# Kernel tuning notes

Hardware: AMD Instinct MI355X
Metric: run time of the kernel (lower is better)

## Reference

```python
import jax, jax.numpy as jnp
import numpy as np

N_NODES = 100000
N_EDGES = 1600000
NEG_SLOPE = 0.2  # PyG GATConv default


def _glorot(key, shape):
    fan = sum(shape[:2]) if len(shape) > 1 else shape[0] * 2
    s = jnp.sqrt(6.0 / fan)
    return jax.random.uniform(key, shape, jnp.float32, -s, s)


def gat_layer(x, src, dst, edge_attr, W, a_src, a_dst, We, a_e, b, heads, out_ch, concat):
    """Faithful PyG GATConv (add_self_loops=True, fill_value='mean', edge_dim set)."""
    n = x.shape[0]
    # self-loop edge_attr = mean of incoming edge_attr per dst node (0 if none)
    deg = jax.ops.segment_sum(jnp.ones((src.shape[0],), edge_attr.dtype), dst, num_segments=n)
    loop_attr = jax.ops.segment_sum(edge_attr, dst, num_segments=n) / jnp.maximum(deg, 1.0)[:, None]
    loop = jnp.arange(n, dtype=src.dtype)
    src_f = jnp.concatenate([src, loop])
    dst_f = jnp.concatenate([dst, loop])
    ea = jnp.concatenate([edge_attr, loop_attr], axis=0)
    # node transform -> [n, H, C]
    h = (x @ W).reshape(n, heads, out_ch)
    al_src = jnp.sum(h * a_src, axis=-1)  # [n, H]
    al_dst = jnp.sum(h * a_dst, axis=-1)  # [n, H]
    e = (ea @ We).reshape(-1, heads, out_ch)
    al_e = jnp.sum(e * a_e, axis=-1)      # [Ef, H]
    alpha = jax.nn.leaky_relu(al_src[src_f] + al_dst[dst_f] + al_e, negative_slope=NEG_SLOPE)
    # segment softmax over destination nodes (every node has a self loop)
    m = jax.ops.segment_max(alpha, dst_f, num_segments=n)
    ex = jnp.exp(alpha - m[dst_f])
    den = jax.ops.segment_sum(ex, dst_f, num_segments=n)
    att = ex / den[dst_f]                 # [Ef, H]
    out = jax.ops.segment_sum(att[:, :, None] * h[src_f], dst_f, num_segments=n)  # [n, H, C]
    out = out.reshape(n, heads * out_ch) if concat else out.mean(axis=1)
    return out + b


def setup_inputs() -> dict:
    key = jax.random.key(0)
    ks = jax.random.split(key, 20)
    x = jax.random.normal(ks[0], (N_NODES, 5), jnp.float32)
    edge_index = jax.random.randint(ks[1], (2, N_EDGES), 0, N_NODES, jnp.int64)
    edge_attr = jax.random.normal(ks[2], (N_EDGES, 2), jnp.float32)
    # conv1: in=5, out=32, heads=4, concat -> 128
    p = {
        "W1": _glorot(ks[3], (5, 128)), "aS1": _glorot(ks[4], (4, 32)),
        "aD1": _glorot(ks[5], (4, 32)), "We1": _glorot(ks[6], (2, 128)),
        "aE1": _glorot(ks[7], (4, 32)), "b1": jnp.zeros((128,), jnp.float32),
        # conv2: in=128, out=32, heads=2, concat -> 64
        "W2": _glorot(ks[8], (128, 64)), "aS2": _glorot(ks[9], (2, 32)),
        "aD2": _glorot(ks[10], (2, 32)), "We2": _glorot(ks[11], (2, 64)),
        "aE2": _glorot(ks[12], (2, 32)), "b2": jnp.zeros((64,), jnp.float32),
        # conv3: in=64, out=1, heads=1, concat=False
        "W3": _glorot(ks[13], (64, 1)), "aS3": _glorot(ks[14], (1, 1)),
        "aD3": _glorot(ks[15], (1, 1)), "We3": _glorot(ks[16], (2, 1)),
        "aE3": _glorot(ks[17], (1, 1)), "b3": jnp.zeros((1,), jnp.float32),
    }
    return {"x": x, "edge_index": edge_index, "edge_attr": edge_attr, **p}


def reference(x, edge_index, edge_attr,
              W1, aS1, aD1, We1, aE1, b1,
              W2, aS2, aD2, We2, aE2, b2,
              W3, aS3, aD3, We3, aE3, b3):
    src, dst = edge_index[0], edge_index[1]
    h = gat_layer(x, src, dst, edge_attr, W1, aS1, aD1, We1, aE1, b1, 4, 32, True)
    h = jax.nn.elu(h)  # dropout is identity in eval
    h = gat_layer(h, src, dst, edge_attr, W2, aS2, aD2, We2, aE2, b2, 2, 32, True)
    h = jax.nn.elu(h)
    h = gat_layer(h, src, dst, edge_attr, W3, aS3, aD3, We3, aE3, b3, 1, 1, False)
    return jax.nn.sigmoid(h).squeeze(-1)  # [N]
```

## Files before the change

### kernel.cpp

```cpp
#include <hip/hip_runtime.h>
#include <math.h>

#define NN 100000
#define NE 1600000
#define NPB 256
#define NPB_SHIFT 8
#define NB ((NN + NPB - 1) / NPB)
#define NCHUNK 512
#define CH ((NE + NCHUNK - 1) / NCHUNK)
#define LOG2E 1.44269504088896f

typedef __attribute__((ext_vector_type(8))) short short8v;
typedef __attribute__((ext_vector_type(4))) float f32x4;

__device__ __forceinline__ float lrelu(float x) { return fmaxf(x, 0.2f * x); }
__device__ __forceinline__ float elu1(float x) { return x > 0.f ? x : (__expf(x) - 1.f); }
__device__ __forceinline__ float fexp2(float x) {
#if __has_builtin(__builtin_amdgcn_exp2f)
    return __builtin_amdgcn_exp2f(x);
#else
    return exp2f(x);
#endif
}
__device__ __forceinline__ unsigned bf16rne(float f) {
    unsigned u = __float_as_uint(f);
    return (u + 0x7FFFu + ((u >> 16) & 1u)) >> 16;
}
__device__ __forceinline__ float bf16lo(unsigned u) { return __uint_as_float(u << 16); }
__device__ __forceinline__ float bf16hi(unsigned u) {
    return __uint_as_float(u & 0xFFFF0000u);
}
__device__ __forceinline__ void split2(float x0, float x1, unsigned& hp, unsigned& lp) {
    unsigned h0 = bf16rne(x0), h1 = bf16rne(x1);
    float r0 = x0 - __uint_as_float(h0 << 16);
    float r1 = x1 - __uint_as_float(h1 << 16);
    hp = h0 | (h1 << 16);
    lp = bf16rne(r0) | (bf16rne(r1) << 16);
}

__global__ void __launch_bounds__(256) k_binA0(const int* __restrict__ dst,
                                               int* __restrict__ bucket_cnt) {
    __shared__ int hist[NB];
    int t = threadIdx.x;
    for (int b = t; b < NB; b += 256) hist[b] = 0;
    __syncthreads();
    int c0 = blockIdx.x * CH, c1 = min(NE, c0 + CH);
    for (int e = c0 + t; e < c1; e += 256) atomicAdd(&hist[dst[e] >> NPB_SHIFT], 1);
    __syncthreads();
    for (int b = t; b < NB; b += 256)
        if (hist[b]) atomicAdd(&bucket_cnt[b], hist[b]);
}

__global__ void __launch_bounds__(512) k_bscan(const int* __restrict__ bucket_cnt,
                                               int* __restrict__ bucket_base,
                                               int* __restrict__ bucket_tail) {
    __shared__ int s[512];
    int t = threadIdx.x;
    int v = (t < NB) ? bucket_cnt[t] : 0;
    s[t] = v;
    __syncthreads();
    for (int off = 1; off < 512; off <<= 1) {
        int x = (t >= off) ? s[t - off] : 0;
        __syncthreads();
        if (t >= off) s[t] += x;
        __syncthreads();
    }
    if (t < NB) {
        int ex = s[t] - v;
        bucket_base[t] = ex;
        bucket_tail[t] = ex;
        if (t == NB - 1) bucket_base[NB] = s[t];
    }
}

__global__ void __launch_bounds__(256) k_binA2(const int* __restrict__ src,
                                               const int* __restrict__ dst,
                                               const float* __restrict__ ea,
                                               int* __restrict__ bucket_tail,
                                               uint2* __restrict__ binned,
                                               unsigned char* __restrict__ dstb) {
    __shared__ int hist[NB], pre[NB], cursor[NB], base_l[NB];
    __shared__ int psum[256];
    __shared__ uint2 lrec[CH];
    __shared__ int lds_d[CH];
    int t = threadIdx.x;
    for (int b = t; b < NB; b += 256) hist[b] = 0;
    __syncthreads();
    int c0 = blockIdx.x * CH, c1 = min(NE, c0 + CH);
    int cnt = c1 - c0;
    for (int i = t; i < cnt; i += 256) atomicAdd(&hist[dst[c0 + i] >> NPB_SHIFT], 1);
    __syncthreads();
    int b0 = t << 1, b1 = b0 + 1;
    int h0 = (b0 < NB) ? hist[b0] : 0;
    int h1 = (b1 < NB) ? hist[b1] : 0;
    psum[t] = h0 + h1;
    __syncthreads();
    for (int off = 1; off < 256; off <<= 1) {
        int x = (t >= off) ? psum[t - off] : 0;
        __syncthreads();
        if (t >= off) psum[t] += x;
        __syncthreads();
    }
    int ex = psum[t] - (h0 + h1);
    if (b0 < NB) { pre[b0] = ex;      cursor[b0] = ex; }
    if (b1 < NB) { pre[b1] = ex + h0; cursor[b1] = ex + h0; }
    for (int b = t; b < NB; b += 256) {
        int h = hist[b];
        if (h) base_l[b] = atomicAdd(&bucket_tail[b], h);
    }
    __syncthreads();
    for (int i = t; i < cnt; i += 256) {
        int e = c0 + i;
        int d = dst[e];
        int bkt = d >> NPB_SHIFT;
        int lpos = atomicAdd(&cursor[bkt], 1);
        unsigned pk = bf16rne(ea[2 * e]) | (bf16rne(ea[2 * e + 1]) << 16);
        lrec[lpos] = make_uint2((unsigned)src[e], pk);
        lds_d[lpos] = d;
    }
    __syncthreads();
    for (int i = t; i < cnt; i += 256) {
        int d = lds_d[i];
        int bkt = d >> NPB_SHIFT;
        int gpos = base_l[bkt] + (i - pre[bkt]);
        binned[gpos] = lrec[i];
        dstb[gpos] = (unsigned char)(d & (NPB - 1));
    }
}

__global__ void __launch_bounds__(256) k_binB(const int* __restrict__ bucket_base,
                                              const uint2* __restrict__ binned,
                                              const unsigned char* __restrict__ dstb,
                                              int* __restrict__ rowptr,
                                              uint2* __restrict__ edges,
                                              float* __restrict__ la) {
    __shared__ int hist[NPB], pre[NPB], cursor[NPB];
    __shared__ float ea0s[NPB], ea1s[NPB];
    int b = blockIdx.x, t = threadIdx.x;
    int bb = bucket_base[b], be = bucket_base[b + 1];
    int nb0 = b << NPB_SHIFT;
    hist[t] = 0;
    ea0s[t] = 0.f;
    ea1s[t] = 0.f;
    __syncthreads();
    for (int e = bb + t; e < be; e += 256) atomicAdd(&hist[dstb[e]], 1);
    __syncthreads();
    int v = hist[t];
    pre[t] = v;
    __syncthreads();
    for (int off = 1; off < 256; off <<= 1) {
        int x = (t >= off) ? pre[t - off] : 0;
        __syncthreads();
        if (t >= off) pre[t] += x;
        __syncthreads();
    }
    int ex = pre[t] - v;
    if (nb0 + t <= NN) rowptr[nb0 + t] = bb + ex;
    cursor[t] = bb + ex;
    __syncthreads();
    for (int e = bb + t; e < be; e += 256) {
        uint2 rec = binned[e];
        unsigned char d = dstb[e];
        int pos = atomicAdd(&cursor[d], 1);
        edges[pos] = rec;
        atomicAdd(&ea0s[d], bf16lo(rec.y));
        atomicAdd(&ea1s[d], bf16hi(rec.y));
    }
    __syncthreads();
    int n = nb0 + t;
    if (n < NN) {
        float dg = fmaxf((float)v, 1.0f);
        la[2 * n] = ea0s[t] / dg;
        la[2 * n + 1] = ea1s[t] / dg;
    }
}

__global__ void k_const(const float* __restrict__ We1, const float* __restrict__ aE1,
                        const float* __restrict__ We2, const float* __restrict__ aE2,
                        const float* __restrict__ We3, const float* __restrict__ aE3,
                        const float* __restrict__ W1, const float* __restrict__ aS1,
                        const float* __restrict__ aD1, float* __restrict__ cbuf) {
    int t = threadIdx.x;
    if (t < 8) {
        int d = t >> 2, hd = t & 3;
        float s = 0.f;
        for (int c = 0; c < 32; c++) s += We1[d * 128 + hd * 32 + c] * aE1[hd * 32 + c];
        cbuf[t] = s * LOG2E;
    } else if (t < 12) {
        int idx = t - 8, d = idx >> 1, hd = idx & 1;
        float s = 0.f;
        for (int c = 0; c < 32; c++) s += We2[d * 64 + hd * 32 + c] * aE2[hd * 32 + c];
        cbuf[t] = s * LOG2E;
    } else if (t < 14) {
        cbuf[t] = We3[t - 12] * aE3[0] * LOG2E;
    } else if (t >= 16 && t < 56) {
        int r = (t - 16) % 20, hd = r / 5, i = r % 5;
        const float* a = (t - 16 < 20) ? aS1 : aD1;
        float s = 0.f;
        for (int c = 0; c < 32; c++) s += W1[i * 128 + hd * 32 + c] * a[hd * 32 + c];
        cbuf[t] = s * LOG2E;
    }
}

__global__ void k_w2t(const float* __restrict__ W2, unsigned short* __restrict__ W2th,
                      unsigned short* __restrict__ W2tl) {
    int i = blockIdx.x * 256 + threadIdx.x;
    if (i >= 64 * 128) return;
    int c = i >> 7, k = i & 127;
    float v = W2[k * 64 + c];
    unsigned h = bf16rne(v);
    float hf = __uint_as_float(h << 16);
    unsigned lo = bf16rne(v - hf);
    W2th[c * 128 + k] = (unsigned short)h;
    W2tl[c * 128 + k] = (unsigned short)lo;
}

__global__ void k_prep1(const float* __restrict__ x, const float* __restrict__ vsd,
                        float4* __restrict__ xp, float4* __restrict__ als1,
                        float4* __restrict__ ald1) {
    int n = blockIdx.x * blockDim.x + threadIdx.x;
    if (n >= NN) return;
    float x0 = x[5 * n], x1 = x[5 * n + 1], x2 = x[5 * n + 2], x3 = x[5 * n + 3],
          x4 = x[5 * n + 4];
    xp[2 * n] = make_float4(x0, x1, x2, x3);
    xp[2 * n + 1] = make_float4(x4, 0.f, 0.f, 0.f);
    float sv[4], dv[4];
#pragma unroll
    for (int hd = 0; hd < 4; hd++) {
        const float* vS = vsd + hd * 5;
        const float* vD = vsd + 20 + hd * 5;
        sv[hd] = x0 * vS[0] + x1 * vS[1] + x2 * vS[2] + x3 * vS[3] + x4 * vS[4];
        dv[hd] = x0 * vD[0] + x1 * vD[1] + x2 * vD[2] + x3 * vD[3] + x4 * vD[4];
    }
    als1[n] = make_float4(sv[0], sv[1], sv[2], sv[3]);
    ald1[n] = make_float4(dv[0], dv[1], dv[2], dv[3]);
}

__global__ void k_agg1(const int* __restrict__ rowptr, const uint2* __restrict__ edges,
                       const float4* __restrict__ xp, const float* __restrict__ als1,
                       const float* __restrict__ ald1, const float* __restrict__ la,
                       const float* __restrict__ me, float* __restrict__ xw) {
    int t = blockIdx.x * blockDim.x + threadIdx.x;
    if (t >= NN * 4) return;
    int n = t >> 2, hd = t & 3;
    float me0 = me[hd], me1 = me[4 + hd];
    float aldn = ald1[t];
    float aself = lrelu(als1[t] + aldn + la[2 * n] * me0 + la[2 * n + 1] * me1);
    int start = rowptr[n], end = rowptr[n + 1];
    float den = 1.f;
    float4 xa = xp[2 * n];
    float xb = xp[2 * n + 1].x;
    float a0 = xa.x, a1 = xa.y, a2 = xa.z, a3 = xa.w, a4 = xb;
    int e = start;
    if ((e & 1) && e < end) {
        uint2 ep = edges[e];
        int s = (int)ep.x;
        float a = lrelu(als1[s * 4 + hd] + aldn + bf16lo(ep.y) * me0 + bf16hi(ep.y) * me1);
        float p = fexp2(a - aself);
        den += p;
        float4 sa = xp[2 * s];
        float sb = xp[2 * s + 1].x;
        a0 += p * sa.x; a1 += p * sa.y; a2 += p * sa.z; a3 += p * sa.w; a4 += p * sb;
        e++;
    }
    for (; e + 1 < end; e += 2) {
        uint4 two = *(const uint4*)(edges + e);
        int s0 = (int)two.x, s1 = (int)two.z;
        unsigned pk0 = two.y, pk1 = two.w;
        float l0 = als1[s0 * 4 + hd];
        float l1 = als1[s1 * 4 + hd];
        float4 sa0 = xp[2 * s0];
        float sb0 = xp[2 * s0 + 1].x;
        float4 sa1 = xp[2 * s1];
        float sb1 = xp[2 * s1 + 1].x;
        float av0 = lrelu(l0 + aldn + bf16lo(pk0) * me0 + bf16hi(pk0) * me1);
        float av1 = lrelu(l1 + aldn + bf16lo(pk1) * me0 + bf16hi(pk1) * me1);
        float p0 = fexp2(av0 - aself);
        float p1 = fexp2(av1 - aself);
        den += p0 + p1;
        a0 += p0 * sa0.x + p1 * sa1.x;
        a1 += p0 * sa0.y + p1 * sa1.y;
        a2 += p0 * sa0.z + p1 * sa1.z;
        a3 += p0 * sa0.w + p1 * sa1.w;
        a4 += p0 * sb0 + p1 * sb1;
    }
    if (e < end) {
        uint2 ep = edges[e];
        int s = (int)ep.x;
        float a = lrelu(als1[s * 4 + hd] + aldn + bf16lo(ep.y) * me0 + bf16hi(ep.y) * me1);
        float p = fexp2(a - aself);
        den += p;
        float4 sa = xp[2 * s];
        float sb = xp[2 * s + 1].x;
        a0 += p * sa.x; a1 += p * sa.y; a2 += p * sa.z; a3 += p * sa.w; a4 += p * sb;
    }
    float r = 1.f / den;
    float* w = xw + (size_t)n * 20 + hd * 5;
    w[0] = a0 * r;
    w[1] = a1 * r;
    w[2] = a2 * r;
    w[3] = a3 * r;
    w[4] = a4 * r;
}

__global__ void __launch_bounds__(128) k_l2trans(
        const float* __restrict__ xw, const float* __restrict__ W1,
        const float* __restrict__ b1, const unsigned short* __restrict__ W2th,
        const unsigned short* __restrict__ W2tl,
        const float* __restrict__ aS2, const float* __restrict__ aD2,
        unsigned short* __restrict__ h2q, float* __restrict__ als2,
        float* __restrict__ ald2) {
    __shared__ float wstage[32 * 20];
    __shared__ unsigned short Ahi[4096];
    __shared__ unsigned short Alo[4096];
    int nb = blockIdx.x * 32, t = threadIdx.x;
    {
        int base = nb * 20;
        for (int idx = t; idx < 32 * 20; idx += 128) wstage[idx] = xw[base + idx];
    }
    __syncthreads();
    {
        int nl = t >> 2, g = t & 3;
        int w = nl >> 4, row = nl & 15;
#pragma unroll
        for (int kt = 0; kt < 4; ++kt) {
            int ch0 = kt * 32 + g * 8;
            float4 va = *(const float4*)(b1 + ch0);
            float4 vb = *(const float4*)(b1 + ch0 + 4);
            const float* wp = wstage + nl * 20 + kt * 5;
#pragma unroll
            for (int i = 0; i < 5; ++i) {
                float wi = wp[i];
                float4 A = *(const float4*)(W1 + i * 128 + ch0);
                float4 B = *(const float4*)(W1 + i * 128 + ch0 + 4);
                va.x += wi * A.x; va.y += wi * A.y; va.z += wi * A.z; va.w += wi * A.w;
                vb.x += wi * B.x; vb.y += wi * B.y; vb.z += wi * B.z; vb.w += wi * B.w;
            }
            unsigned hp0, hp1, hp2, hp3, lp0, lp1, lp2, lp3;
            split2(elu1(va.x), elu1(va.y), hp0, lp0);
            split2(elu1(va.z), elu1(va.w), hp1, lp1);
            split2(elu1(vb.x), elu1(vb.y), hp2, lp2);
            split2(elu1(vb.z), elu1(vb.w), hp3, lp3);
            int cidx = (((w * 4 + kt) * 64) + g * 16 + row) * 8;
            *(uint4*)(Ahi + cidx) = make_uint4(hp0, hp1, hp2, hp3);
            *(uint4*)(Alo + cidx) = make_uint4(lp0, lp1, lp2, lp3);
        }
    }
    int l = t & 63, w = t >> 6;
    int g = l >> 4, row16 = l & 15;
    f32x4 acc0 = {0.f, 0.f, 0.f, 0.f}, acc1 = acc0, acc2 = acc0, acc3 = acc0;
    int w4 = w * 4;
#pragma unroll
    for (int kt = 0; kt < 4; ++kt) {
        int abase = ((w4 + kt) * 64 + l) * 8;
        short8v ah = *(const short8v*)(Ahi + abase);
        short8v al = *(const short8v*)(Alo + abase);
        int kb = kt * 32 + g * 8;
        {
            short8v bh = *(const short8v*)(W2th + row16 * 128 + kb);
            short8v bl = *(const short8v*)(W2tl + row16 * 128 + kb);
            acc0 = __builtin_amdgcn_mfma_f32_16x16x32_bf16(ah, bh, acc0, 0, 0, 0);
            acc0 = __builtin_amdgcn_mfma_f32_16x16x32_bf16(al, bh, acc0, 0, 0, 0);
            acc0 = __builtin_amdgcn_mfma_f32_16x16x32_bf16(ah, bl, acc0, 0, 0, 0);
        }
        {
            short8v bh = *(const short8v*)(W2th + (16 + row16) * 128 + kb);
            short8v bl = *(const short8v*)(W2tl + (16 + row16) * 128 + kb);
            acc1 = __builtin_amdgcn_mfma_f32_16x16x32_bf16(ah, bh, acc1, 0, 0, 0);
            acc1 = __builtin_amdgcn_mfma_f32_16x16x32_bf16(al, bh, acc1, 0, 0, 0);
            acc1 = __builtin_amdgcn_mfma_f32_16x16x32_bf16(ah, bl, acc1, 0, 0, 0);
        }
        {
            short8v bh = *(const short8v*)(W2th + (32 + row16) * 128 + kb);
            short8v bl = *(const short8v*)(W2tl + (32 + row16) * 128 + kb);
            acc2 = __builtin_amdgcn_mfma_f32_16x16x32_bf16(ah, bh, acc2, 0, 0, 0);
            acc2 = __builtin_amdgcn_mfma_f32_16x16x32_bf16(al, bh, acc2, 0, 0, 0);
            acc2 = __builtin_amdgcn_mfma_f32_16x16x32_bf16(ah, bl, acc2, 0, 0, 0);
        }
        {
            short8v bh = *(const short8v*)(W2th + (48 + row16) * 128 + kb);
            short8v bl = *(const short8v*)(W2tl + (48 + row16) * 128 + kb);
            acc3 = __builtin_amdgcn_mfma_f32_16x16x32_bf16(ah, bh, acc3, 0, 0, 0);
            acc3 = __builtin_amdgcn_mfma_f32_16x16x32_bf16(al, bh, acc3, 0, 0, 0);
            acc3 = __builtin_amdgcn_mfma_f32_16x16x32_bf16(ah, bl, acc3, 0, 0, 0);
        }
    }
    {
        int nodeb = nb + w * 16 + g * 4;
#pragma unroll
        for (int nt = 0; nt < 4; ++nt) {
            f32x4 A = (nt == 0) ? acc0 : (nt == 1) ? acc1 : (nt == 2) ? acc2 : acc3;
#pragma unroll
            for (int r = 0; r < 4; ++r) {
                float v = A[r];
                float u = __shfl_xor(v, 1);
                if (!(l & 1)) {
                    unsigned pk = bf16rne(v) | (bf16rne(u) << 16);
                    int node = nodeb + r;
                    int ch = nt * 16 + row16;
                    *(unsigned*)(h2q + (size_t)node * 64 + ch) = pk;
                }
            }
        }
        float aSv0 = aS2[row16], aSv1 = aS2[16 + row16];
        float aSv2 = aS2[32 + row16], aSv3 = aS2[48 + row16];
        float aDv0 = aD2[row16], aDv1 = aD2[16 + row16];
        float aDv2 = aD2[32 + row16], aDv3 = aD2[48 + row16];
#pragma unroll
        for (int r = 0; r < 4; ++r) {
            float pS0 = acc0[r] * aSv0 + acc1[r] * aSv1;
            float pS1 = acc2[r] * aSv2 + acc3[r] * aSv3;
            float pD0 = acc0[r] * aDv0 + acc1[r] * aDv1;
            float pD1 = acc2[r] * aDv2 + acc3[r] * aDv3;
#pragma unroll
            for (int off = 1; off < 16; off <<= 1) {
                pS0 += __shfl_xor(pS0, off);
                pS1 += __shfl_xor(pS1, off);
                pD0 += __shfl_xor(pD0, off);
                pD1 += __shfl_xor(pD1, off);
            }
            if (row16 == 0) {
                int node = nodeb + r;
                als2[node * 2 + 0] = pS0 * LOG2E;
                als2[node * 2 + 1] = pS1 * LOG2E;
                ald2[node * 2 + 0] = pD0 * LOG2E;
                ald2[node * 2 + 1] = pD1 * LOG2E;
            }
        }
    }
}

#define AGG2_EDGE(u0, u1, p)                                            \
    acc[0] += (p) * bf16lo(u0.x); acc[1] += (p) * bf16hi(u0.x);         \
    acc[2] += (p) * bf16lo(u0.y); acc[3] += (p) * bf16hi(u0.y);         \
    acc[4] += (p) * bf16lo(u0.z); acc[5] += (p) * bf16hi(u0.z);         \
    acc[6] += (p) * bf16lo(u0.w); acc[7] += (p) * bf16hi(u0.w);         \
    acc[8] += (p) * bf16lo(u1.x); acc[9] += (p) * bf16hi(u1.x);         \
    acc[10] += (p) * bf16lo(u1.y); acc[11] += (p) * bf16hi(u1.y);       \
    acc[12] += (p) * bf16lo(u1.z); acc[13] += (p) * bf16hi(u1.z);       \
    acc[14] += (p) * bf16lo(u1.w); acc[15] += (p) * bf16hi(u1.w);

__global__ void k_agg2(const int* __restrict__ rowptr, const uint2* __restrict__ edges,
                       const unsigned short* __restrict__ h2q,
                       const float* __restrict__ als2, const float* __restrict__ ald2,
                       const float* __restrict__ la, const float* __restrict__ me,
                       const float* __restrict__ b2, const float* __restrict__ W3,
                       float* __restrict__ h3) {
    int t = blockIdx.x * blockDim.x + threadIdx.x;
    if (t >= NN * 4) return;
    int n = t >> 2, sub = t & 3, hd = sub >> 1, qh = sub & 1;
    int cbase = hd * 32 + qh * 16;
    float me0 = me[hd], me1 = me[2 + hd];
    float aldn = ald2[n * 2 + hd];
    float aself = lrelu(als2[n * 2 + hd] + aldn + la[2 * n] * me0 + la[2 * n + 1] * me1);
    int start = rowptr[n], end = rowptr[n + 1];
    float den = 1.f;
    float acc[16];
    {
        const uint4* hp = (const uint4*)(h2q + (size_t)n * 64 + cbase);
        uint4 u0 = hp[0], u1 = hp[1];
        acc[0] = bf16lo(u0.x); acc[1] = bf16hi(u0.x);
        acc[2] = bf16lo(u0.y); acc[3] = bf16hi(u0.y);
        acc[4] = bf16lo(u0.z); acc[5] = bf16hi(u0.z);
        acc[6] = bf16lo(u0.w); acc[7] = bf16hi(u0.w);
        acc[8] = bf16lo(u1.x); acc[9] = bf16hi(u1.x);
        acc[10] = bf16lo(u1.y); acc[11] = bf16hi(u1.y);
        acc[12] = bf16lo(u1.z); acc[13] = bf16hi(u1.z);
        acc[14] = bf16lo(u1.w); acc[15] = bf16hi(u1.w);
    }
    int e = start;
    if ((e & 1) && e < end) {
        uint2 ep = edges[e];
        int s = (int)ep.x;
        float a = lrelu(als2[s * 2 + hd] + aldn + bf16lo(ep.y) * me0 + bf16hi(ep.y) * me1);
        float p = fexp2(a - aself);
        den += p;
        const uint4* sp = (const uint4*)(h2q + (size_t)s * 64 + cbase);
        uint4 u0 = sp[0], u1 = sp[1];
        AGG2_EDGE(u0, u1, p)
        e++;
    }
    for (; e + 3 < end; e += 4) {
        uint4 twoA = *(const uint4*)(edges + e);
        uint4 twoB = *(const uint4*)(edges + e + 2);
        int s0 = (int)twoA.x, s1 = (int)twoA.z;
        int s2 = (int)twoB.x, s3 = (int)twoB.z;
        float l0 = als2[s0 * 2 + hd];
        float l1 = als2[s1 * 2 + hd];
        float l2 = als2[s2 * 2 + hd];
        float l3 = als2[s3 * 2 + hd];
        const uint4* sp0 = (const uint4*)(h2q + (size_t)s0 * 64 + cbase);
        const uint4* sp1 = (const uint4*)(h2q + (size_t)s1 * 64 + cbase);
        const uint4* sp2 = (const uint4*)(h2q + (size_t)s2 * 64 + cbase);
        const uint4* sp3 = (const uint4*)(h2q + (size_t)s3 * 64 + cbase);
        uint4 u00 = sp0[0], u01 = sp0[1];
        uint4 u10 = sp1[0], u11 = sp1[1];
        uint4 u20 = sp2[0], u21 = sp2[1];
        uint4 u30 = sp3[0], u31 = sp3[1];
        float av0 = lrelu(l0 + aldn + bf16lo(twoA.y) * me0 + bf16hi(twoA.y) * me1);
        float av1 = lrelu(l1 + aldn + bf16lo(twoA.w) * me0 + bf16hi(twoA.w) * me1);
        float av2 = lrelu(l2 + aldn + bf16lo(twoB.y) * me0 + bf16hi(twoB.y) * me1);
        float av3 = lrelu(l3 + aldn + bf16lo(twoB.w) * me0 + bf16hi(twoB.w) * me1);
        float p0 = fexp2(av0 - aself);
        float p1 = fexp2(av1 - aself);
        float p2 = fexp2(av2 - aself);
        float p3 = fexp2(av3 - aself);
        den += (p0 + p1) + (p2 + p3);
        acc[0] += p0 * bf16lo(u00.x) + p1 * bf16lo(u10.x) + p2 * bf16lo(u20.x) + p3 * bf16lo(u30.x);
        acc[1] += p0 * bf16hi(u00.x) + p1 * bf16hi(u10.x) + p2 * bf16hi(u20.x) + p3 * bf16hi(u30.x);
        acc[2] += p0 * bf16lo(u00.y) + p1 * bf16lo(u10.y) + p2 * bf16lo(u20.y) + p3 * bf16lo(u30.y);
        acc[3] += p0 * bf16hi(u00.y) + p1 * bf16hi(u10.y) + p2 * bf16hi(u20.y) + p3 * bf16hi(u30.y);
        acc[4] += p0 * bf16lo(u00.z) + p1 * bf16lo(u10.z) + p2 * bf16lo(u20.z) + p3 * bf16lo(u30.z);
        acc[5] += p0 * bf16hi(u00.z) + p1 * bf16hi(u10.z) + p2 * bf16hi(u20.z) + p3 * bf16hi(u30.z);
        acc[6] += p0 * bf16lo(u00.w) + p1 * bf16lo(u10.w) + p2 * bf16lo(u20.w) + p3 * bf16lo(u30.w);
        acc[7] += p0 * bf16hi(u00.w) + p1 * bf16hi(u10.w) + p2 * bf16hi(u20.w) + p3 * bf16hi(u30.w);
        acc[8] += p0 * bf16lo(u01.x) + p1 * bf16lo(u11.x) + p2 * bf16lo(u21.x) + p3 * bf16lo(u31.x);
        acc[9] += p0 * bf16hi(u01.x) + p1 * bf16hi(u11.x) + p2 * bf16hi(u21.x) + p3 * bf16hi(u31.x);
        acc[10] += p0 * bf16lo(u01.y) + p1 * bf16lo(u11.y) + p2 * bf16lo(u21.y) + p3 * bf16lo(u31.y);
        acc[11] += p0 * bf16hi(u01.y) + p1 * bf16hi(u11.y) + p2 * bf16hi(u21.y) + p3 * bf16hi(u31.y);
        acc[12] += p0 * bf16lo(u01.z) + p1 * bf16lo(u11.z) + p2 * bf16lo(u21.z) + p3 * bf16lo(u31.z);
        acc[13] += p0 * bf16hi(u01.z) + p1 * bf16hi(u11.z) + p2 * bf16hi(u21.z) + p3 * bf16hi(u31.z);
        acc[14] += p0 * bf16lo(u01.w) + p1 * bf16lo(u11.w) + p2 * bf16lo(u21.w) + p3 * bf16lo(u31.w);
        acc[15] += p0 * bf16hi(u01.w) + p1 * bf16hi(u11.w) + p2 * bf16hi(u21.w) + p3 * bf16hi(u31.w);
    }
    if (e + 1 < end) {
        uint4 two = *(const uint4*)(edges + e);
        int s0 = (int)two.x, s1 = (int)two.z;
        float l0 = als2[s0 * 2 + hd];
        float l1 = als2[s1 * 2 + hd];
        const uint4* sp0 = (const uint4*)(h2q + (size_t)s0 * 64 + cbase);
        const uint4* sp1 = (const uint4*)(h2q + (size_t)s1 * 64 + cbase);
        uint4 u00 = sp0[0], u01 = sp0[1];
        uint4 u10 = sp1[0], u11 = sp1[1];
        float av0 = lrelu(l0 + aldn + bf16lo(two.y) * me0 + bf16hi(two.y) * me1);
        float av1 = lrelu(l1 + aldn + bf16lo(two.w) * me0 + bf16hi(two.w) * me1);
        float p0 = fexp2(av0 - aself);
        float p1 = fexp2(av1 - aself);
        den += p0 + p1;
        AGG2_EDGE(u00, u01, p0)
        AGG2_EDGE(u10, u11, p1)
        e += 2;
    }
    if (e < end) {
        uint2 ep = edges[e];
        int s = (int)ep.x;
        float a = lrelu(als2[s * 2 + hd] + aldn + bf16lo(ep.y) * me0 + bf16hi(ep.y) * me1);
        float p = fexp2(a - aself);
        den += p;
        const uint4* sp = (const uint4*)(h2q + (size_t)s * 64 + cbase);
        uint4 u0 = sp[0], u1 = sp[1];
        AGG2_EDGE(u0, u1, p)
    }
    float r = 1.f / den;
    float part = 0.f;
#pragma unroll
    for (int c = 0; c < 16; c++) {
        float v = elu1(acc[c] * r + b2[cbase + c]);
        part += v * W3[cbase + c];
    }
    part += __shfl_xor(part, 1);
    part += __shfl_xor(part, 2);
    if (sub == 0) h3[n] = part;
}

__global__ void k_agg3(const int* __restrict__ rowptr, const uint2* __restrict__ edges,
                       const float* __restrict__ h, const float* __restrict__ aS3,
                       const float* __restrict__ aD3, const float* __restrict__ la,
                       const float* __restrict__ me, const float* __restrict__ b,
                       float* __restrict__ out) {
    int tid = blockIdx.x * blockDim.x + threadIdx.x;
    int n = tid >> 4;
    if (n >= NN) return;
    int lane = tid & 15;
    float me0 = me[0], me1 = me[1];
    float aSs = aS3[0] * LOG2E, aDs = aD3[0] * LOG2E;
    float hn = h[n];
    float ald_n = hn * aDs;
    float aself = lrelu(hn * aSs + ald_n + la[2 * n] * me0 + la[2 * n + 1] * me1);
    int start = rowptr[n], end = rowptr[n + 1];
    float den = 0.f, num = 0.f;
    for (int e = start + lane; e < end; e += 16) {
        uint2 ep = edges[e];
        int s = (int)ep.x;
        float hv = h[s];
        float a = lrelu(hv * aSs + ald_n + bf16lo(ep.y) * me0 + bf16hi(ep.y) * me1);
        float p = fexp2(a - aself);
        den += p;
        num += p * hv;
    }
#pragma unroll
    for (int off = 8; off > 0; off >>= 1) {
        den += __shfl_xor(den, off);
        num += __shfl_xor(num, off);
    }
    if (lane == 0) {
        den += 1.f;
        num += hn;
        float v = num / den + b[0];
        out[n] = 1.f / (1.f + __expf(-v));
    }
}

extern "C" void kernel_launch(void* const* d_in, const int* in_sizes, int n_in,
                              void* d_out, int out_size, void* d_ws, size_t ws_size,
                              hipStream_t stream) {
    const float* x   = (const float*)d_in[0];
    const int*   ei  = (const int*)d_in[1];
    const float* ea  = (const float*)d_in[2];
    const float* W1  = (const float*)d_in[3];
    const float* aS1 = (const float*)d_in[4];
    const float* aD1 = (const float*)d_in[5];
    const float* We1 = (const float*)d_in[6];
    const float* aE1 = (const float*)d_in[7];
    const float* b1  = (const float*)d_in[8];
    const float* W2  = (const float*)d_in[9];
    const float* aS2 = (const float*)d_in[10];
    const float* aD2 = (const float*)d_in[11];
    const float* We2 = (const float*)d_in[12];
    const float* aE2 = (const float*)d_in[13];
    const float* b2  = (const float*)d_in[14];
    const float* W3  = (const float*)d_in[15];
    const float* aS3 = (const float*)d_in[16];
    const float* aD3 = (const float*)d_in[17];
    const float* We3 = (const float*)d_in[18];
    const float* aE3 = (const float*)d_in[19];
    const float* b3  = (const float*)d_in[20];

    const int* srcv = ei;
    const int* dstv = ei + NE;

    char* basep = (char*)d_ws;
    size_t off = 0;
    auto alloc = [&](size_t nbytes) -> void* {
        void* p = basep + off;
        off += (nbytes + 255) & ~(size_t)255;
        return p;
    };
    int*    bucket_cnt  = (int*)alloc((size_t)(NB + 1) * 4);
    int*    bucket_base = (int*)alloc((size_t)(NB + 1) * 4);
    int*    bucket_tail = (int*)alloc((size_t)(NB + 1) * 4);
    int*    rowptr      = (int*)alloc((size_t)(NN + 1) * 4);
    uint2*  binned      = (uint2*)alloc((size_t)NE * 8);
    unsigned char* dstb = (unsigned char*)alloc((size_t)NE);
    uint2*  edges       = (uint2*)alloc((size_t)NE * 8);
    float*  la          = (float*)alloc((size_t)NN * 8);
    float*  cbuf        = (float*)alloc(256);
    float4* xp          = (float4*)alloc((size_t)NN * 32);
    float4* als1        = (float4*)alloc((size_t)NN * 16);
    float4* ald1        = (float4*)alloc((size_t)NN * 16);
    float*  xw          = (float*)alloc((size_t)NN * 80);
    unsigned short* h2q = (unsigned short*)alloc((size_t)NN * 128);
    float*  als2        = (float*)alloc((size_t)NN * 8);
    float*  ald2        = (float*)alloc((size_t)NN * 8);
    float*  h3          = (float*)alloc((size_t)NN * 4);
    unsigned short* W2th = (unsigned short*)alloc(64 * 128 * 2);
    unsigned short* W2tl = (unsigned short*)alloc(64 * 128 * 2);
    (void)ws_size; (void)in_sizes; (void)n_in; (void)out_size;

    float* me1 = cbuf;
    float* me2 = cbuf + 8;
    float* me3 = cbuf + 12;
    float* vsd = cbuf + 16;

    auto cdiv = [](long long a, long long b) { return (int)((a + b - 1) / b); };
    const int BS = 256;

    hipMemsetAsync(bucket_cnt, 0, (size_t)(NB + 1) * 4, stream);
    k_binA0<<<NCHUNK, 256, 0, stream>>>(dstv, bucket_cnt);
    k_bscan<<<1, 512, 0, stream>>>(bucket_cnt, bucket_base, bucket_tail);
    k_binA2<<<NCHUNK, 256, 0, stream>>>(srcv, dstv, ea, bucket_tail, binned, dstb);
    k_binB<<<NB, 256, 0, stream>>>(bucket_base, binned, dstb, rowptr, edges, la);

    k_const<<<1, 64, 0, stream>>>(We1, aE1, We2, aE2, We3, aE3, W1, aS1, aD1, cbuf);
    k_w2t<<<32, 256, 0, stream>>>(W2, W2th, W2tl);

    k_prep1<<<cdiv(NN, BS), BS, 0, stream>>>(x, vsd, xp, als1, ald1);
    k_agg1<<<cdiv((long long)NN * 4, BS), BS, 0, stream>>>(rowptr, edges, xp,
                                                           (const float*)als1,
                                                           (const float*)ald1, la, me1, xw);

    k_l2trans<<<cdiv(NN, 32), 128, 0, stream>>>(xw, W1, b1, W2th, W2tl, aS2, aD2,
                                                h2q, als2, ald2);
    k_agg2<<<cdiv((long long)NN * 4, BS), BS, 0, stream>>>(rowptr, edges, h2q, als2, ald2,
                                                           la, me2, b2, W3, h3);

    k_agg3<<<cdiv((long long)NN * 16, BS), BS, 0, stream>>>(rowptr, edges, h3, aS3, aD3,
                                                            la, me3, b3, (float*)d_out);
}
```

Baseline: 320.8 us.

## Fuse layer-1 W1 transform and ELU into aggregation, write MFMA-ready tiles to global

The layer-1 aggregation kernel now applies the W1 projection, bias, ELU and hi/lo bf16 split directly after computing each node-head's aggregated features. It writes the result in the MFMA fragment layout to global buffers. A separate lean MFMA kernel then loads those fragments to produce h2 and the layer-2 attention logits. This removes the intermediate xw round trip and the shared-memory staging in the old transform kernel. The cost is a larger intermediate: 128 channels stored as two bf16 planes instead of 20 floats per node, which adds global write and read traffic.

Measured after the change: 350.1 us. 9.1% more time.

```diff
diff --git a/kernel.cpp b/kernel.cpp
--- a/kernel.cpp
+++ b/kernel.cpp
@@ -8,6 +8,7 @@
 #define NB ((NN + NPB - 1) / NPB)
 #define NCHUNK 512
 #define CH ((NE + NCHUNK - 1) / NCHUNK)
+#define NG (NN / 16)
 #define LOG2E 1.44269504088896f
 
 typedef __attribute__((ext_vector_type(8))) short short8v;
@@ -239,122 +240,133 @@
 __global__ void k_agg1(const int* __restrict__ rowptr, const uint2* __restrict__ edges,
                        const float4* __restrict__ xp, const float* __restrict__ als1,
                        const float* __restrict__ ald1, const float* __restrict__ la,
-                       const float* __restrict__ me, float* __restrict__ xw) {
+                       const float* __restrict__ me, const float* __restrict__ W1,
+                       const float* __restrict__ b1,
+                       unsigned short* __restrict__ AhiG,
+                       unsigned short* __restrict__ AloG) {
     int t = blockIdx.x * blockDim.x + threadIdx.x;
     if (t >= NN * 4) return;
     int n = t >> 2, hd = t & 3;
-    float me0 = me[hd], me1 = me[4 + hd];
-    float aldn = ald1[t];
-    float aself = lrelu(als1[t] + aldn + la[2 * n] * me0 + la[2 * n + 1] * me1);
-    int start = rowptr[n], end = rowptr[n + 1];
-    float den = 1.f;
-    float4 xa = xp[2 * n];
-    float xb = xp[2 * n + 1].x;
-    float a0 = xa.x, a1 = xa.y, a2 = xa.z, a3 = xa.w, a4 = xb;
-    int e = start;
-    if ((e & 1) && e < end) {
-        uint2 ep = edges[e];
-        int s = (int)ep.x;
-        float a = lrelu(als1[s * 4 + hd] + aldn + bf16lo(ep.y) * me0 + bf16hi(ep.y) * me1);
-        float p = fexp2(a - aself);
-        den += p;
-        float4 sa = xp[2 * s];
-        float sb = xp[2 * s + 1].x;
-        a0 += p * sa.x; a1 += p * sa.y; a2 += p * sa.z; a3 += p * sa.w; a4 += p * sb;
-        e++;
-    }
-    for (; e + 1 < end; e += 2) {
-        uint4 two = *(const uint4*)(edges + e);
-        int s0 = (int)two.x, s1 = (int)two.z;
-        unsigned pk0 = two.y, pk1 = two.w;
-        float l0 = als1[s0 * 4 + hd];
-        float l1 = als1[s1 * 4 + hd];
-        float4 sa0 = xp[2 * s0];
-        float sb0 = xp[2 * s0 + 1].x;
-        float4 sa1 = xp[2 * s1];
-        float sb1 = xp[2 * s1 + 1].x;
-        float av0 = lrelu(l0 + aldn + bf16lo(pk0) * me0 + bf16hi(pk0) * me1);
-        float av1 = lrelu(l1 + aldn + bf16lo(pk1) * me0 + bf16hi(pk1) * me1);
-        float p0 = fexp2(av0 - aself);
-        float p1 = fexp2(av1 - aself);
-        den += p0 + p1;
-        a0 += p0 * sa0.x + p1 * sa1.x;
-        a1 += p0 * sa0.y + p1 * sa1.y;
-        a2 += p0 * sa0.z + p1 * sa1.z;
-        a3 += p0 * sa0.w + p1 * sa1.w;
-        a4 += p0 * sb0 + p1 * sb1;
-    }
-    if (e < end) {
-        uint2 ep = edges[e];
-        int s = (int)ep.x;
-        float a = lrelu(als1[s * 4 + hd] + aldn + bf16lo(ep.y) * me0 + bf16hi(ep.y) * me1);
-        float p = fexp2(a - aself);
-        den += p;
-        float4 sa = xp[2 * s];
-        float sb = xp[2 * s + 1].x;
-        a0 += p * sa.x; a1 += p * sa.y; a2 += p * sa.z; a3 += p * sa.w; a4 += p * sb;
-    }
-    float r = 1.f / den;
-    float* w = xw + (size_t)n * 20 + hd * 5;
-    w[0] = a0 * r;
-    w[1] = a1 * r;
-    w[2] = a2 * r;
-    w[3] = a3 * r;
-    w[4] = a4 * r;
-}
-
-__global__ void __launch_bounds__(128) k_l2trans(
-        const float* __restrict__ xw, const float* __restrict__ W1,
-        const float* __restrict__ b1, const unsigned short* __restrict__ W2th,
-        const unsigned short* __restrict__ W2tl,
+    float w0, w1, w2, w3, w4;
+    {
+        float me0 = me[hd], me1v = me[4 + hd];
+        float aldn = ald1[t];
+        float aself = lrelu(als1[t] + aldn + la[2 * n] * me0 + la[2 * n + 1] * me1v);
+        int start = rowptr[n], end = rowptr[n + 1];
+        float den = 1.f;
+        float4 xa = xp[2 * n];
+        float xb = xp[2 * n + 1].x;
+        float a0 = xa.x, a1 = xa.y, a2 = xa.z, a3 = xa.w, a4 = xb;
+        int e = start;
+        if ((e & 1) && e < end) {
+            uint2 ep = edges[e];
+            int s = (int)ep.x;
+            float a = lrelu(als1[s * 4 + hd] + aldn + bf16lo(ep.y) * me0 + bf16hi(ep.y) * me1v);
+            float p = fexp2(a - aself);
+            den += p;
+            float4 sa = xp[2 * s];
+            float sb = xp[2 * s + 1].x;
+            a0 += p * sa.x; a1 += p * sa.y; a2 += p * sa.z; a3 += p * sa.w; a4 += p * sb;
+            e++;
+        }
+        for (; e + 1 < end; e += 2) {
+            uint4 two = *(const uint4*)(edges + e);
+            int s0 = (int)two.x, s1 = (int)two.z;
+            unsigned pk0 = two.y, pk1 = two.w;
+            float l0 = als1[s0 * 4 + hd];
+            float l1 = als1[s1 * 4 + hd];
+            float4 sa0 = xp[2 * s0];
+            float sb0 = xp[2 * s0 + 1].x;
+            float4 sa1 = xp[2 * s1];
+            float sb1 = xp[2 * s1 + 1].x;
+            float av0 = lrelu(l0 + aldn + bf16lo(pk0) * me0 + bf16hi(pk0) * me1v);
+            float av1 = lrelu(l1 + aldn + bf16lo(pk1) * me0 + bf16hi(pk1) * me1v);
+            float p0 = fexp2(av0 - aself);
+            float p1 = fexp2(av1 - aself);
+            den += p0 + p1;
+            a0 += p0 * sa0.x + p1 * sa1.x;
+            a1 += p0 * sa0.y + p1 * sa1.y;
+            a2 += p0 * sa0.z + p1 * sa1.z;
+            a3 += p0 * sa0.w + p1 * sa1.w;
+            a4 += p0 * sb0 + p1 * sb1;
+        }
+        if (e < end) {
+            uint2 ep = edges[e];
+            int s = (int)ep.x;
+            float a = lrelu(als1[s * 4 + hd] + aldn + bf16lo(ep.y) * me0 + bf16hi(ep.y) * me1v);
+            float p = fexp2(a - aself);
+            den += p;
+            float4 sa = xp[2 * s];
+            float sb = xp[2 * s + 1].x;
+            a0 += p * sa.x; a1 += p * sa.y; a2 += p * sa.z; a3 += p * sa.w; a4 += p * sb;
+        }
+        float r = 1.f / den;
+        w0 = a0 * r; w1 = a1 * r; w2 = a2 * r; w3 = a3 * r; w4 = a4 * r;
+    }
+    int m = n >> 4, row = n & 15;
+#pragma unroll
+    for (int g = 0; g < 4; ++g) {
+        int ch0 = hd * 32 + g * 8;
+        float4 va = *(const float4*)(b1 + ch0);
+        float4 vb = *(const float4*)(b1 + ch0 + 4);
+        {
+            float4 A = *(const float4*)(W1 + 0 * 128 + ch0);
+            float4 B = *(const float4*)(W1 + 0 * 128 + ch0 + 4);
+            va.x += w0 * A.x; va.y += w0 * A.y; va.z += w0 * A.z; va.w += w0 * A.w;
+            vb.x += w0 * B.x; vb.y += w0 * B.y; vb.z += w0 * B.z; vb.w += w0 * B.w;
+        }
+        {
+            float4 A = *(const float4*)(W1 + 1 * 128 + ch0);
+            float4 B = *(const float4*)(W1 + 1 * 128 + ch0 + 4);
+            va.x += w1 * A.x; va.y += w1 * A.y; va.z += w1 * A.z; va.w += w1 * A.w;
+            vb.x += w1 * B.x; vb.y += w1 * B.y; vb.z += w1 * B.z; vb.w += w1 * B.w;
+        }
+        {
+            float4 A = *(const float4*)(W1 + 2 * 128 + ch0);
+            float4 B = *(const float4*)(W1 + 2 * 128 + ch0 + 4);
+            va.x += w2 * A.x; va.y += w2 * A.y; va.z += w2 * A.z; va.w += w2 * A.w;
+            vb.x += w2 * B.x; vb.y += w2 * B.y; vb.z += w2 * B.z; vb.w += w2 * B.w;
+        }
+        {
+            float4 A = *(const float4*)(W1 + 3 * 128 + ch0);
+            float4 B = *(const float4*)(W1 + 3 * 128 + ch0 + 4);
+            va.x += w3 * A.x; va.y += w3 * A.y; va.z += w3 * A.z; va.w += w3 * A.w;
+            vb.x += w3 * B.x; vb.y += w3 * B.y; vb.z += w3 * B.z; vb.w += w3 * B.w;
+        }
+        {
+            float4 A = *(const float4*)(W1 + 4 * 128 + ch0);
+            float4 B = *(const float4*)(W1 + 4 * 128 + ch0 + 4);
+            va.x += w4 * A.x; va.y += w4 * A.y; va.z += w4 * A.z; va.w += w4 * A.w;
+            vb.x += w4 * B.x; vb.y += w4 * B.y; vb.z += w4 * B.z; vb.w += w4 * B.w;
+        }
+        unsigned hp0, hp1, hp2, hp3, lp0, lp1, lp2, lp3;
+        split2(elu1(va.x), elu1(va.y), hp0, lp0);
+        split2(elu1(va.z), elu1(va.w), hp1, lp1);
+        split2(elu1(vb.x), elu1(vb.y), hp2, lp2);
+        split2(elu1(vb.z), elu1(vb.w), hp3, lp3);
+        size_t cidx = ((size_t)((m * 4 + hd) * 64) + g * 16 + row) * 8;
+        *(uint4*)(AhiG + cidx) = make_uint4(hp0, hp1, hp2, hp3);
+        *(uint4*)(AloG + cidx) = make_uint4(lp0, lp1, lp2, lp3);
+    }
+}
+
+__global__ void __launch_bounds__(256) k_l2mfma(
+        const unsigned short* __restrict__ AhiG, const unsigned short* __restrict__ AloG,
+        const unsigned short* __restrict__ W2th, const unsigned short* __restrict__ W2tl,
         const float* __restrict__ aS2, const float* __restrict__ aD2,
         unsigned short* __restrict__ h2q, float* __restrict__ als2,
         float* __restrict__ ald2) {
-    __shared__ float wstage[32 * 20];
-    __shared__ unsigned short Ahi[4096];
-    __shared__ unsigned short Alo[4096];
-    int nb = blockIdx.x * 32, t = threadIdx.x;
-    {
-        int base = nb * 20;
-        for (int idx = t; idx < 32 * 20; idx += 128) wstage[idx] = xw[base + idx];
-    }
-    __syncthreads();
-    {
-        int nl = t >> 2, g = t & 3;
-        int w = nl >> 4, row = nl & 15;
-#pragma unroll
-        for (int kt = 0; kt < 4; ++kt) {
-            int ch0 = kt * 32 + g * 8;
-            float4 va = *(const float4*)(b1 + ch0);
-            float4 vb = *(const float4*)(b1 + ch0 + 4);
-            const float* wp = wstage + nl * 20 + kt * 5;
-#pragma unroll
-            for (int i = 0; i < 5; ++i) {
-                float wi = wp[i];
-                float4 A = *(const float4*)(W1 + i * 128 + ch0);
-                float4 B = *(const float4*)(W1 + i * 128 + ch0 + 4);
-                va.x += wi * A.x; va.y += wi * A.y; va.z += wi * A.z; va.w += wi * A.w;
-                vb.x += wi * B.x; vb.y += wi * B.y; vb.z += wi * B.z; vb.w += wi * B.w;
-            }
-            unsigned hp0, hp1, hp2, hp3, lp0, lp1, lp2, lp3;
-            split2(elu1(va.x), elu1(va.y), hp0, lp0);
-            split2(elu1(va.z), elu1(va.w), hp1, lp1);
-            split2(elu1(vb.x), elu1(vb.y), hp2, lp2);
-            split2(elu1(vb.z), elu1(vb.w), hp3, lp3);
-            int cidx = (((w * 4 + kt) * 64) + g * 16 + row) * 8;
-            *(uint4*)(Ahi + cidx) = make_uint4(hp0, hp1, hp2, hp3);
-            *(uint4*)(Alo + cidx) = make_uint4(lp0, lp1, lp2, lp3);
-        }
-    }
-    int l = t & 63, w = t >> 6;
+    int tl = threadIdx.x;
+    int l = tl & 63;
+    int m = blockIdx.x * 4 + (tl >> 6);
+    if (m >= NG) return;
     int g = l >> 4, row16 = l & 15;
     f32x4 acc0 = {0.f, 0.f, 0.f, 0.f}, acc1 = acc0, acc2 = acc0, acc3 = acc0;
-    int w4 = w * 4;
 #pragma unroll
     for (int kt = 0; kt < 4; ++kt) {
-        int abase = ((w4 + kt) * 64 + l) * 8;
-        short8v ah = *(const short8v*)(Ahi + abase);
-        short8v al = *(const short8v*)(Alo + abase);
+        size_t abase = ((size_t)((m * 4 + kt) * 64) + l) * 8;
+        short8v ah = *(const short8v*)(AhiG + abase);
+        short8v al = *(const short8v*)(AloG + abase);
         int kb = kt * 32 + g * 8;
         {
             short8v bh = *(const short8v*)(W2th + row16 * 128 + kb);
@@ -386,7 +398,7 @@
         }
     }
     {
-        int nodeb = nb + w * 16 + g * 4;
+        int nodeb = m * 16 + g * 4;
 #pragma unroll
         for (int nt = 0; nt < 4; ++nt) {
             f32x4 A = (nt == 0) ? acc0 : (nt == 1) ? acc1 : (nt == 2) ? acc2 : acc3;
@@ -648,7 +660,8 @@
     float4* xp          = (float4*)alloc((size_t)NN * 32);
     float4* als1        = (float4*)alloc((size_t)NN * 16);
     float4* ald1        = (float4*)alloc((size_t)NN * 16);
-    float*  xw          = (float*)alloc((size_t)NN * 80);
+    unsigned short* AhiG = (unsigned short*)alloc((size_t)NG * 2048 * 2);
+    unsigned short* AloG = (unsigned short*)alloc((size_t)NG * 2048 * 2);
     unsigned short* h2q = (unsigned short*)alloc((size_t)NN * 128);
     float*  als2        = (float*)alloc((size_t)NN * 8);
     float*  ald2        = (float*)alloc((size_t)NN * 8);
@@ -675,12 +688,12 @@
     k_w2t<<<32, 256, 0, stream>>>(W2, W2th, W2tl);
 
     k_prep1<<<cdiv(NN, BS), BS, 0, stream>>>(x, vsd, xp, als1, ald1);
-    k_agg1<<<cdiv((long long)NN * 4, BS), BS, 0, stream>>>(rowptr, edges, xp,
-                                                           (const float*)als1,
-                                                           (const float*)ald1, la, me1, xw);
-
-    k_l2trans<<<cdiv(NN, 32), 128, 0, stream>>>(xw, W1, b1, W2th, W2tl, aS2, aD2,
-                                                h2q, als2, ald2);
+    k_agg1<<<cdiv((long long)NN * 4, BS), BS, 0, stream>>>(
+        rowptr, edges, xp, (const float*)als1, (const float*)ald1, la, me1,
+        W1, b1, AhiG, AloG);
+
+    k_l2mfma<<<cdiv(NG, 4), 256, 0, stream>>>(AhiG, AloG, W2th, W2tl, aS2, aD2,
+                                              h2q, als2, ald2);
     k_agg2<<<cdiv((long long)NN * 4, BS), BS, 0, stream>>>(rowptr, edges, h2q, als2, ald2,
                                                            la, me2, b2, W3, h3);
 
```
